# Performance work log

Hardware: AMD Instinct MI355X
Metric: run time of the kernel (lower is better)

The kernel has to match this reference:

```python
import jax, jax.numpy as jnp
import numpy as np
import math

D_MODEL = 768
N_HEADS = 12
HEAD_DIM = D_MODEL // N_HEADS
B, T = 2, 4096


def setup_inputs() -> dict:
    key = jax.random.key(0)
    k1, k2, k3, k4 = jax.random.split(key, 4)
    x = jax.random.normal(k1, (B, T, D_MODEL), dtype=jnp.float32)
    mask = jax.random.randint(k2, (B, T), 0, 2).astype(jnp.bool_)
    # torch Linear init scale ~ 1/sqrt(fan_in); use scaled normal for stability
    w_qkv = jax.random.normal(k3, (3 * D_MODEL, D_MODEL), dtype=jnp.float32) / math.sqrt(D_MODEL)
    w_proj = jax.random.normal(k4, (D_MODEL, D_MODEL), dtype=jnp.float32) / math.sqrt(D_MODEL)
    b_proj = jnp.zeros((D_MODEL,), dtype=jnp.float32)
    return {"x": x, "mask": mask, "w_qkv": w_qkv, "w_proj": w_proj, "b_proj": b_proj}


def reference(x, mask, w_qkv, w_proj, b_proj):
    Bb, Tt, D = x.shape
    H, Hd = N_HEADS, HEAD_DIM
    scale = math.sqrt(Hd)
    # qkv projection (bias-free): (B,T,3D) -> (3,B,H,T,Hd)
    qkv = jnp.einsum('btd,ed->bte', x, w_qkv)
    qkv = qkv.reshape(Bb, Tt, 3, H, Hd).transpose(2, 0, 3, 1, 4)
    q, k, v = qkv[0], qkv[1], qkv[2]
    # full T x T scores (faithful to non-fused original)
    attn = jnp.einsum('bhqd,bhkd->bhqk', q, k) / scale
    attn = jnp.where(mask[:, None, None, :], -jnp.inf, attn)
    attn = jax.nn.softmax(attn, axis=-1)  # dropout p=0 -> identity
    out = jnp.einsum('bhqk,bhkd->bhqd', attn, v)
    out = out.transpose(0, 2, 1, 3).reshape(Bb, Tt, D)
    return jnp.einsum('btd,ed->bte', out, w_proj) + b_proj
```

## Files before the change

kernel.cpp:

```cpp
#include <hip/hip_runtime.h>

#define D_MODEL 768
#define N_HEADS 12
#define SEQ 4096
#define KVB 64

typedef __attribute__((ext_vector_type(4))) float f32x4;
typedef __attribute__((ext_vector_type(16))) float f32x16;
typedef __attribute__((ext_vector_type(8))) short bf16x8;
typedef __attribute__((ext_vector_type(4))) unsigned short u16x4;

typedef __attribute__((address_space(3))) void lds_void;
typedef __attribute__((address_space(1))) const void glb_void;

static __device__ __forceinline__ void gld_lds16(const void* g, void* l) {
    __builtin_amdgcn_global_load_lds((glb_void*)g, (lds_void*)l, 16, 0, 0);
}

static __device__ __forceinline__ unsigned short f32_bf16(float f) {
    union { float f; unsigned int u; } c; c.f = f;
    unsigned int u = c.u;
    u += 0x7FFFu + ((u >> 16) & 1u);
    return (unsigned short)(u >> 16);
}

static __device__ __forceinline__ unsigned int cvtpk(float lo, float hi) {
    unsigned int r;
    asm("v_cvt_pk_bf16_f32 %0, %1, %2" : "=v"(r) : "v"(lo), "v"(hi));
    return r;
}

__global__ void cvt_bf16(const float* __restrict__ in, unsigned short* __restrict__ out, int n) {
    int i = (blockIdx.x * blockDim.x + threadIdx.x) * 4;
    int stride = gridDim.x * blockDim.x * 4;
    for (; i < n; i += stride) {
        f32x4 v = *(const f32x4*)(in + i);
        u16x4 o;
        o[0] = f32_bf16(v[0]); o[1] = f32_bf16(v[1]);
        o[2] = f32_bf16(v[2]); o[3] = f32_bf16(v[3]);
        *(u16x4*)(out + i) = o;
    }
}

__global__ __launch_bounds__(256) void qkv_gemm(const unsigned short* __restrict__ A,
                                                const unsigned short* __restrict__ Bw,
                                                unsigned short* __restrict__ qb,
                                                unsigned short* __restrict__ kb,
                                                unsigned short* __restrict__ vb) {
    __shared__ __attribute__((aligned(16))) unsigned short lA[128*32];
    __shared__ __attribute__((aligned(16))) unsigned short lB[128*32];
    const int K = 768;
    int tid = threadIdx.x;
    int wave = tid >> 6, lane = tid & 63;
    int qr = (wave >> 1) * 64, qc = (wave & 1) * 64;
    int m0 = blockIdx.x * 128, n0 = blockIdx.y * 128;
    f32x4 acc[4][4] = {};
    int c0 = tid * 2;

    for (int kt = 0; kt < K; kt += 32) {
        __syncthreads();
        #pragma unroll
        for (int i = 0; i < 2; ++i) {
            int c = c0 + i;
            int row = c >> 2, col = (c & 3) * 8;
            *(bf16x8*)&lA[row*32 + col] = *(const bf16x8*)(A  + (size_t)(m0 + row) * K + kt + col);
            *(bf16x8*)&lB[row*32 + col] = *(const bf16x8*)(Bw + (size_t)(n0 + row) * K + kt + col);
        }
        __syncthreads();
        bf16x8 af[4], bfr[4];
        #pragma unroll
        for (int m = 0; m < 4; ++m)
            af[m] = *(bf16x8*)&lA[(qr + m*16 + (lane & 15))*32 + (lane >> 4)*8];
        #pragma unroll
        for (int n = 0; n < 4; ++n)
            bfr[n] = *(bf16x8*)&lB[(qc + n*16 + (lane & 15))*32 + (lane >> 4)*8];
        #pragma unroll
        for (int m = 0; m < 4; ++m)
            #pragma unroll
            for (int n = 0; n < 4; ++n)
                acc[m][n] = __builtin_amdgcn_mfma_f32_16x16x32_bf16(af[m], bfr[n], acc[m][n], 0, 0, 0);
    }
    #pragma unroll
    for (int n = 0; n < 4; ++n) {
        int colg = n0 + qc + n*16 + (lane & 15);
        int s = colg / 768;
        int rem = colg - s * 768;
        int h = rem >> 6, d = rem & 63;
        if (s == 2) {
            #pragma unroll
            for (int m = 0; m < 4; ++m) {
                int rowb = m0 + qr + m*16 + (lane >> 4)*4;
                int bb = rowb >> 12, t0 = rowb & 4095;
                u16x4 pk;
                #pragma unroll
                for (int r = 0; r < 4; ++r) pk[r] = f32_bf16(acc[m][n][r]);
                *(u16x4*)(vb + ((size_t)((bb*12 + h)*64 + d))*4096 + t0) = pk;
            }
        } else {
            unsigned short* dst = (s == 0) ? qb : kb;
            float scl = (s == 0) ? 0.125f : 1.0f;
            #pragma unroll
            for (int m = 0; m < 4; ++m) {
                int rowb = m0 + qr + m*16 + (lane >> 4)*4;
                #pragma unroll
                for (int r = 0; r < 4; ++r) {
                    int row = rowb + r;
                    int bb = row >> 12, t = row & 4095;
                    dst[((size_t)((bb*12 + h)*4096 + t))*64 + d] = f32_bf16(acc[m][n][r] * scl);
                }
            }
        }
    }
}

__global__ __launch_bounds__(512, 4) void attn_kern(const unsigned short* __restrict__ qbuf,
                                                    const unsigned short* __restrict__ kbuf,
                                                    const unsigned short* __restrict__ vtbuf,
                                                    const int* __restrict__ mask,
                                                    unsigned short* __restrict__ ob) {
    __shared__ __attribute__((aligned(16))) char lds[2][16384];
    __shared__ float lds_l[4][32];

    const int tid = threadIdx.x, wave = tid >> 6, lane = tid & 63;
    const int l31 = lane & 31, hi2 = lane >> 5;
    const int lane16 = lane * 16;
    const int wq = wave & 3, wk = wave >> 2;

    int raw = blockIdx.x;
    int sb = (raw & 7) * 96 + (raw >> 3);
    int bh = sb >> 5, qi = sb & 31;
    int q0 = qi * 128;
    int b = bh / 12, h = bh - b*12;

    const unsigned short* Qb = qbuf + (size_t)bh * SEQ * 64;
    const unsigned short* Kb = kbuf + (size_t)bh * SEQ * 64;
    const unsigned short* Vt = vtbuf + (size_t)bh * 64 * SEQ;
    const int* mrow = mask + b * SEQ;

    bf16x8 bq[4];
    #pragma unroll
    for (int ds = 0; ds < 4; ++ds)
        bq[ds] = *(const bf16x8*)(Qb + (size_t)(q0 + wq*32 + l31)*64 + ds*16 + hi2*8);

    union U4 { unsigned int w[4]; bf16x8 v; };
    U4 bext; bext.w[0] = (hi2 == 0) ? 0x3F80u : 0u; bext.w[1] = bext.w[2] = bext.w[3] = 0u;

    auto stage = [&](char* buf, int kv0) {
        #pragma unroll
        for (int i = 0; i < 2; ++i) {
            int fi = wave*2 + i;
            const unsigned short* gsrc;
            if (fi < 8) {
                int kt = fi >> 2, ds = fi & 3;
                gsrc = Kb + (size_t)(kv0 + kt*32 + l31)*64 + ds*16 + hi2*8;
            } else {
                int g = fi - 8, dt = g >> 2, ks = g & 3;
                gsrc = Vt + (size_t)(dt*32 + l31)*4096 + kv0 + ks*16 + hi2*8;
            }
            gld_lds16(gsrc, buf + fi*1024);
        }
    };

    f32x16 oacc0 = {}, oacc1 = {};
    float lr = 0.0f;

    stage(lds[0], 0);
    int mb = mrow[wk*32 + l31];
    __syncthreads();

    const int NT = SEQ / KVB;
    for (int t = 0; t < NT; ++t) {
        int kv0 = t * KVB;
        char* bufK = lds[t & 1];
        char* bufV = bufK + 8192;
        int mbn = 0;
        if (t + 1 < NT) {
            stage(lds[(t + 1) & 1], kv0 + KVB);
            mbn = mrow[kv0 + KVB + wk*32 + l31];
        }

        U4 ab;
        ab.w[0] = (hi2 == 0) ? (mb ? 0xC6EAu : 0xC140u) : 0u;
        ab.w[1] = ab.w[2] = ab.w[3] = 0u;

        f32x16 s = {};
        s = __builtin_amdgcn_mfma_f32_32x32x16_bf16(ab.v, bext.v, s, 0, 0, 0);
        #pragma unroll
        for (int ds = 0; ds < 4; ++ds) {
            bf16x8 aK = *(bf16x8*)(bufK + (wk*4 + ds)*1024 + lane16);
            s = __builtin_amdgcn_mfma_f32_32x32x16_bf16(aK, bq[ds], s, 0, 0, 0);
        }

        float rs = 0.0f;
        #pragma unroll
        for (int i = 0; i < 16; ++i) { s[i] = __expf(s[i]); rs += s[i]; }
        rs += __shfl_xor(rs, 32);
        lr += rs;

        bool ishi = (hi2 != 0);
        bf16x8 pa[2];
        #pragma unroll
        for (int sb2 = 0; sb2 < 2; ++sb2) {
            unsigned int X0 = cvtpk(s[8*sb2+0], s[8*sb2+1]);
            unsigned int X1 = cvtpk(s[8*sb2+2], s[8*sb2+3]);
            unsigned int Y0 = cvtpk(s[8*sb2+4], s[8*sb2+5]);
            unsigned int Y1 = cvtpk(s[8*sb2+6], s[8*sb2+7]);
            unsigned int s0 = ishi ? X0 : Y0, s1 = ishi ? X1 : Y1;
            unsigned int r0 = __shfl_xor(s0, 32), r1 = __shfl_xor(s1, 32);
            U4 w;
            w.w[0] = ishi ? r0 : X0;
            w.w[1] = ishi ? r1 : X1;
            w.w[2] = ishi ? Y0 : r0;
            w.w[3] = ishi ? Y1 : r1;
            pa[sb2] = w.v;
        }

        #pragma unroll
        for (int sb2 = 0; sb2 < 2; ++sb2) {
            int ksg = wk*2 + sb2;
            bf16x8 bv0 = *(bf16x8*)(bufV + (0*4 + ksg)*1024 + lane16);
            bf16x8 bv1 = *(bf16x8*)(bufV + (1*4 + ksg)*1024 + lane16);
            oacc0 = __builtin_amdgcn_mfma_f32_32x32x16_bf16(pa[sb2], bv0, oacc0, 0, 0, 0);
            oacc1 = __builtin_amdgcn_mfma_f32_32x32x16_bf16(pa[sb2], bv1, oacc1, 0, 0, 0);
        }

        __syncthreads();
        mb = mbn;
    }

    float* cbase = (float*)lds + wq * 2048;
    if (wk == 1) {
        #pragma unroll
        for (int i = 0; i < 16; ++i) {
            cbase[i*64 + lane]        = oacc0[i];
            cbase[(16 + i)*64 + lane] = oacc1[i];
        }
        if (lane < 32) lds_l[wq][lane] = lr;
    }
    __syncthreads();
    if (wk == 0 && lane < 32) lds_l[wq][lane] += lr;
    __syncthreads();
    if (wk == 0) {
        #pragma unroll
        for (int r = 0; r < 16; ++r) {
            int q = (r & 3) + 8*(r >> 2) + 4*hi2;
            float inv = 1.0f / lds_l[wq][q];
            int tg = q0 + wq*32 + q;
            size_t base = ((size_t)(b*SEQ + tg)) * D_MODEL + h*64 + l31;
            ob[base]      = f32_bf16((oacc0[r] + cbase[r*64 + lane])        * inv);
            ob[base + 32] = f32_bf16((oacc1[r] + cbase[(16 + r)*64 + lane]) * inv);
        }
    }
}

__global__ __launch_bounds__(256) void proj_gemm(const unsigned short* __restrict__ A,
                                                 const unsigned short* __restrict__ Bw,
                                                 const float* __restrict__ bias,
                                                 float* __restrict__ out) {
    __shared__ __attribute__((aligned(16))) unsigned short lA[128*32];
    __shared__ __attribute__((aligned(16))) unsigned short lB[128*32];
    const int K = 768;
    int tid = threadIdx.x;
    int wave = tid >> 6, lane = tid & 63;
    int qr = (wave >> 1) * 64, qc = (wave & 1) * 64;
    int m0 = blockIdx.x * 128, n0 = blockIdx.y * 128;
    f32x4 acc[4][4] = {};
    int c0 = tid * 2;

    for (int kt = 0; kt < K; kt += 32) {
        __syncthreads();
        #pragma unroll
        for (int i = 0; i < 2; ++i) {
            int c = c0 + i;
            int row = c >> 2, col = (c & 3) * 8;
            *(bf16x8*)&lA[row*32 + col] = *(const bf16x8*)(A  + (size_t)(m0 + row) * K + kt + col);
            *(bf16x8*)&lB[row*32 + col] = *(const bf16x8*)(Bw + (size_t)(n0 + row) * K + kt + col);
        }
        __syncthreads();
        bf16x8 af[4], bfr[4];
        #pragma unroll
        for (int m = 0; m < 4; ++m)
            af[m] = *(bf16x8*)&lA[(qr + m*16 + (lane & 15))*32 + (lane >> 4)*8];
        #pragma unroll
        for (int n = 0; n < 4; ++n)
            bfr[n] = *(bf16x8*)&lB[(qc + n*16 + (lane & 15))*32 + (lane >> 4)*8];
        #pragma unroll
        for (int m = 0; m < 4; ++m)
            #pragma unroll
            for (int n = 0; n < 4; ++n)
                acc[m][n] = __builtin_amdgcn_mfma_f32_16x16x32_bf16(af[m], bfr[n], acc[m][n], 0, 0, 0);
    }
    #pragma unroll
    for (int n = 0; n < 4; ++n) {
        int colg = n0 + qc + n*16 + (lane & 15);
        float bn = bias[colg];
        #pragma unroll
        for (int m = 0; m < 4; ++m) {
            int rowb = m0 + qr + m*16 + (lane >> 4)*4;
            #pragma unroll
            for (int r = 0; r < 4; ++r)
                out[(size_t)(rowb + r) * 768 + colg] = acc[m][n][r] + bn;
        }
    }
}

extern "C" void kernel_launch(void* const* d_in, const int* in_sizes, int n_in,
                              void* d_out, int out_size, void* d_ws, size_t ws_size,
                              hipStream_t stream) {
    const float* x      = (const float*)d_in[0];
    const int*   mask   = (const int*)d_in[1];
    const float* w_qkv  = (const float*)d_in[2];
    const float* w_proj = (const float*)d_in[3];
    const float* b_proj = (const float*)d_in[4];
    float* out = (float*)d_out;

    unsigned short* ws = (unsigned short*)d_ws;
    unsigned short* xb     = ws;
    unsigned short* wqkvb  = xb     + 6291456;
    unsigned short* wprojb = wqkvb  + 1769472;
    unsigned short* qb     = wprojb + 589824;
    unsigned short* kb     = qb     + 6291456;
    unsigned short* vtb    = kb     + 6291456;
    unsigned short* ob     = vtb    + 6291456;

    cvt_bf16<<<1024, 256, 0, stream>>>(x,      xb,     6291456);
    cvt_bf16<<<256,  256, 0, stream>>>(w_qkv,  wqkvb,  1769472);
    cvt_bf16<<<128,  256, 0, stream>>>(w_proj, wprojb, 589824);

    qkv_gemm<<<dim3(64, 18), 256, 0, stream>>>(xb, wqkvb, qb, kb, vtb);
    attn_kern<<<768, 512, 0, stream>>>(qb, kb, vtb, mask, ob);
    proj_gemm<<<dim3(64, 6), 256, 0, stream>>>(ob, wprojb, b_proj, out);
}
```

Measured before the change: 260.0 us.

## Use direct global-to-LDS swizzled loads in GEMMs, exp2 softmax, MFMA priority

Both projection GEMMs now stage tiles with global_load_lds instead of going through registers, and use an XOR-swizzled LDS layout so fragment reads avoid bank conflicts. The attention kernel folds log2(e) into the Q scale and the mask bias constants so it can call exp2f in place of __expf. It also raises wave priority around the MFMA sections. The main risks are the swizzle and bf16 constant encodings being subtly wrong, and setprio having little effect.

```diff
diff --git a/kernel.cpp b/kernel.cpp
--- a/kernel.cpp
+++ b/kernel.cpp
@@ -41,6 +41,8 @@
         *(u16x4*)(out + i) = o;
     }
 }
+
+#define QSCL 0.18033688f
 
 __global__ __launch_bounds__(256) void qkv_gemm(const unsigned short* __restrict__ A,
                                                 const unsigned short* __restrict__ Bw,
@@ -55,25 +57,28 @@
     int qr = (wave >> 1) * 64, qc = (wave & 1) * 64;
     int m0 = blockIdx.x * 128, n0 = blockIdx.y * 128;
     f32x4 acc[4][4] = {};
-    int c0 = tid * 2;
+    const int sl = (((lane >> 4) ^ (lane & 3)) * 16);
 
     for (int kt = 0; kt < K; kt += 32) {
         __syncthreads();
         #pragma unroll
         for (int i = 0; i < 2; ++i) {
-            int c = c0 + i;
-            int row = c >> 2, col = (c & 3) * 8;
-            *(bf16x8*)&lA[row*32 + col] = *(const bf16x8*)(A  + (size_t)(m0 + row) * K + kt + col);
-            *(bf16x8*)&lB[row*32 + col] = *(const bf16x8*)(Bw + (size_t)(n0 + row) * K + kt + col);
+            int c = i*256 + tid;
+            int row = c >> 2;
+            int col = ((c & 3) ^ (row & 3)) * 8;
+            char* dA = (char*)lA + (i*256 + wave*64)*16;
+            char* dB = (char*)lB + (i*256 + wave*64)*16;
+            gld_lds16(A  + (size_t)(m0 + row) * K + kt + col, dA);
+            gld_lds16(Bw + (size_t)(n0 + row) * K + kt + col, dB);
         }
         __syncthreads();
         bf16x8 af[4], bfr[4];
         #pragma unroll
         for (int m = 0; m < 4; ++m)
-            af[m] = *(bf16x8*)&lA[(qr + m*16 + (lane & 15))*32 + (lane >> 4)*8];
+            af[m] = *(bf16x8*)((char*)lA + (qr + m*16 + (lane & 15))*64 + sl);
         #pragma unroll
         for (int n = 0; n < 4; ++n)
-            bfr[n] = *(bf16x8*)&lB[(qc + n*16 + (lane & 15))*32 + (lane >> 4)*8];
+            bfr[n] = *(bf16x8*)((char*)lB + (qc + n*16 + (lane & 15))*64 + sl);
         #pragma unroll
         for (int m = 0; m < 4; ++m)
             #pragma unroll
@@ -98,7 +103,7 @@
             }
         } else {
             unsigned short* dst = (s == 0) ? qb : kb;
-            float scl = (s == 0) ? 0.125f : 1.0f;
+            float scl = (s == 0) ? QSCL : 1.0f;
             #pragma unroll
             for (int m = 0; m < 4; ++m) {
                 int rowb = m0 + qr + m*16 + (lane >> 4)*4;
@@ -180,9 +185,10 @@
         }
 
         U4 ab;
-        ab.w[0] = (hi2 == 0) ? (mb ? 0xC6EAu : 0xC140u) : 0u;
+        ab.w[0] = (hi2 == 0) ? (mb ? 0xC480u : 0xC18Au) : 0u;
         ab.w[1] = ab.w[2] = ab.w[3] = 0u;
 
+        __builtin_amdgcn_s_setprio(1);
         f32x16 s = {};
         s = __builtin_amdgcn_mfma_f32_32x32x16_bf16(ab.v, bext.v, s, 0, 0, 0);
         #pragma unroll
@@ -190,10 +196,11 @@
             bf16x8 aK = *(bf16x8*)(bufK + (wk*4 + ds)*1024 + lane16);
             s = __builtin_amdgcn_mfma_f32_32x32x16_bf16(aK, bq[ds], s, 0, 0, 0);
         }
+        __builtin_amdgcn_s_setprio(0);
 
         float rs = 0.0f;
         #pragma unroll
-        for (int i = 0; i < 16; ++i) { s[i] = __expf(s[i]); rs += s[i]; }
+        for (int i = 0; i < 16; ++i) { s[i] = exp2f(s[i]); rs += s[i]; }
         rs += __shfl_xor(rs, 32);
         lr += rs;
 
@@ -215,6 +222,7 @@
             pa[sb2] = w.v;
         }
 
+        __builtin_amdgcn_s_setprio(1);
         #pragma unroll
         for (int sb2 = 0; sb2 < 2; ++sb2) {
             int ksg = wk*2 + sb2;
@@ -223,6 +231,7 @@
             oacc0 = __builtin_amdgcn_mfma_f32_32x32x16_bf16(pa[sb2], bv0, oacc0, 0, 0, 0);
             oacc1 = __builtin_amdgcn_mfma_f32_32x32x16_bf16(pa[sb2], bv1, oacc1, 0, 0, 0);
         }
+        __builtin_amdgcn_s_setprio(0);
 
         __syncthreads();
         mb = mbn;
@@ -265,25 +274,28 @@
     int qr = (wave >> 1) * 64, qc = (wave & 1) * 64;
     int m0 = blockIdx.x * 128, n0 = blockIdx.y * 128;
     f32x4 acc[4][4] = {};
-    int c0 = tid * 2;
+    const int sl = (((lane >> 4) ^ (lane & 3)) * 16);
 
     for (int kt = 0; kt < K; kt += 32) {
         __syncthreads();
         #pragma unroll
         for (int i = 0; i < 2; ++i) {
-            int c = c0 + i;
-            int row = c >> 2, col = (c & 3) * 8;
-            *(bf16x8*)&lA[row*32 + col] = *(const bf16x8*)(A  + (size_t)(m0 + row) * K + kt + col);
-            *(bf16x8*)&lB[row*32 + col] = *(const bf16x8*)(Bw + (size_t)(n0 + row) * K + kt + col);
+            int c = i*256 + tid;
+            int row = c >> 2;
+            int col = ((c & 3) ^ (row & 3)) * 8;
+            char* dA = (char*)lA + (i*256 + wave*64)*16;
+            char* dB = (char*)lB + (i*256 + wave*64)*16;
+            gld_lds16(A  + (size_t)(m0 + row) * K + kt + col, dA);
+            gld_lds16(Bw + (size_t)(n0 + row) * K + kt + col, dB);
         }
         __syncthreads();
         bf16x8 af[4], bfr[4];
         #pragma unroll
         for (int m = 0; m < 4; ++m)
-            af[m] = *(bf16x8*)&lA[(qr + m*16 + (lane & 15))*32 + (lane >> 4)*8];
+            af[m] = *(bf16x8*)((char*)lA + (qr + m*16 + (lane & 15))*64 + sl);
         #pragma unroll
         for (int n = 0; n < 4; ++n)
-            bfr[n] = *(bf16x8*)&lB[(qc + n*16 + (lane & 15))*32 + (lane >> 4)*8];
+            bfr[n] = *(bf16x8*)((char*)lB + (qc + n*16 + (lane & 15))*64 + sl);
         #pragma unroll
         for (int m = 0; m < 4; ++m)
             #pragma unroll
```

After: 280.6 us. +7.9%, slower.
